# Optimization experiments

Hardware: AMD Instinct MI355X
Metric: run time of the kernel (lower is better)

## Reference

```python
import jax, jax.numpy as jnp
import numpy as np

D_MODEL = 2048
NUM_HEADS = 16
D_HEAD = D_MODEL // NUM_HEADS
ROPE_THETA = 10000.0
MAX_SEQ_LEN = 2048
NEG_INF = -1e30


def _rope_tables(seq_len):
    pos = jnp.arange(seq_len, dtype=jnp.float32)[:, None]          # [s,1]
    i = jnp.arange(0, D_HEAD, 2, dtype=jnp.float32)                 # [d/2]
    freqs = 1.0 / (ROPE_THETA ** (i / D_HEAD))
    angles = pos * freqs                                            # [s, d/2]
    return jnp.cos(angles), jnp.sin(angles)


def _apply_rope(x, cos, sin):
    # x: [b,h,s,d]; interleaved pairs: x1 = even dims, x2 = odd dims
    x1 = x[..., 0::2]
    x2 = x[..., 1::2]
    r1 = x1 * cos - x2 * sin
    r2 = x1 * sin + x2 * cos
    return jnp.stack([r1, r2], axis=-1).reshape(x.shape)


def setup_inputs() -> dict:
    key = jax.random.key(0)
    ks = jax.random.split(key, 5)
    b, s = 2, 2048
    scale = 1.0 / np.sqrt(D_MODEL)  # ~kaiming fan_in scale
    return {
        "x": jax.random.normal(ks[0], (b, s, D_MODEL), jnp.float32),
        "Wq": jax.random.normal(ks[1], (D_MODEL, D_MODEL), jnp.float32) * scale,
        "bq": jnp.zeros((D_MODEL,), jnp.float32),
        "Wk": jax.random.normal(ks[2], (D_MODEL, D_MODEL), jnp.float32) * scale,
        "bk": jnp.zeros((D_MODEL,), jnp.float32),
        "Wv": jax.random.normal(ks[3], (D_MODEL, D_MODEL), jnp.float32) * scale,
        "bv": jnp.zeros((D_MODEL,), jnp.float32),
        "Wo": jax.random.normal(ks[4], (D_MODEL, D_MODEL), jnp.float32) * scale,
        "bo": jnp.zeros((D_MODEL,), jnp.float32),
    }


def reference(x, Wq, bq, Wk, bk, Wv, bv, Wo, bo):
    b, s, _ = x.shape
    # QKV projections (torch Linear: y = x @ W.T + b)
    q = x @ Wq.T + bq
    k = x @ Wk.T + bk
    v = x @ Wv.T + bv
    # split heads: b s (h d) -> b h s d
    def split(t):
        return t.reshape(b, s, NUM_HEADS, D_HEAD).transpose(0, 2, 1, 3)
    q, k, v = split(q), split(k), split(v)
    # RoPE
    cos, sin = _rope_tables(s)
    q = _apply_rope(q, cos, sin)
    k = _apply_rope(k, cos, sin)
    # scaled dot-product attention with causal mask
    scores = jnp.einsum('bhqd,bhkd->bhqk', q, k) / jnp.sqrt(jnp.float32(D_HEAD))
    causal = jnp.tril(jnp.ones((s, s), dtype=bool))
    scores = jnp.where(causal[None, None], scores, NEG_INF)
    attn = jax.nn.softmax(scores, axis=-1)
    out = jnp.einsum('bhqk,bhkd->bhqd', attn, v)
    # merge heads and output projection
    out = out.transpose(0, 2, 1, 3).reshape(b, s, D_MODEL)
    return out @ Wo.T + bo
```

## Files before the change

kernel.cpp:

```cpp
#include <hip/hip_runtime.h>
#include <math.h>

#define D_MODEL 2048
#define NH 16
#define DH 128
#define SEQ 2048
#define NBH 32

typedef unsigned short u16;
typedef unsigned int u32;
typedef __attribute__((ext_vector_type(8))) short short8;
typedef __attribute__((ext_vector_type(4))) float floatx4;
typedef __attribute__((ext_vector_type(4))) unsigned short ushort4v;

__device__ __forceinline__ u16 f2bf(float f) {
  u32 u = __builtin_bit_cast(u32, f);
  return (u16)((u + 0x8000u) >> 16);
}
__device__ __forceinline__ float bf2f(u16 h) {
  return __builtin_bit_cast(float, (u32)h << 16);
}

__device__ __forceinline__ void async_load16(const u16* g, u16* l) {
  __builtin_amdgcn_global_load_lds(
      (const __attribute__((address_space(1))) void*)g,
      (__attribute__((address_space(3))) void*)l, 16, 0, 0);
}

template <int CTRL>
__device__ __forceinline__ float dpp_mov(float x) {
  return __builtin_bit_cast(
      float, __builtin_amdgcn_update_dpp(0, __builtin_bit_cast(int, x), CTRL,
                                         0xf, 0xf, false));
}
__device__ __forceinline__ float rmax16(float x) {
  x = fmaxf(x, dpp_mov<0x121>(x));
  x = fmaxf(x, dpp_mov<0x122>(x));
  x = fmaxf(x, dpp_mov<0x124>(x));
  x = fmaxf(x, dpp_mov<0x128>(x));
  return x;
}
__device__ __forceinline__ float radd16(float x) {
  x += dpp_mov<0x121>(x);
  x += dpp_mov<0x122>(x);
  x += dpp_mov<0x124>(x);
  x += dpp_mov<0x128>(x);
  return x;
}

__global__ void cvt_kernel(const float* __restrict__ src, u16* __restrict__ dst,
                           int n) {
  const int i = (blockIdx.x * 256 + threadIdx.x) * 8;
  if (i >= n) return;
  const floatx4 a = *(const floatx4*)(src + i);
  const floatx4 b = *(const floatx4*)(src + i + 4);
  short8 h;
  h[0] = (short)f2bf(a[0]); h[1] = (short)f2bf(a[1]);
  h[2] = (short)f2bf(a[2]); h[3] = (short)f2bf(a[3]);
  h[4] = (short)f2bf(b[0]); h[5] = (short)f2bf(b[1]);
  h[6] = (short)f2bf(b[2]); h[7] = (short)f2bf(b[3]);
  *(short8*)(dst + i) = h;
}

__global__ __launch_bounds__(256, 2) void gemm_async(
    const u16* __restrict__ A, const u16* __restrict__ W0,
    const u16* __restrict__ W1, const u16* __restrict__ W2,
    const float* __restrict__ b0, const float* __restrict__ b1,
    const float* __restrict__ b2, void* __restrict__ C0, void* __restrict__ C1,
    void* __restrict__ C2, const int qkv) {
  __shared__ u16 As[128 * 64];
  __shared__ u16 Bs[128 * 64];
  const int tid = threadIdx.x;
  const int wave = tid >> 6, lane = tid & 63;
  const int lr = lane & 15, lg = lane >> 4;
  const int m0 = blockIdx.y * 128;
  const int wm = (wave & 1) * 64, wn = (wave >> 1) * 64;

  int n0, mode;
  const u16* W;
  const float* bias;
  void* C;
  if (qkv) {
    const int which = blockIdx.x >> 4;
    n0 = (blockIdx.x & 15) * 128;
    W = which == 0 ? W0 : which == 1 ? W1 : W2;
    bias = which == 0 ? b0 : which == 1 ? b1 : b2;
    C = which == 0 ? C0 : which == 1 ? C1 : C2;
    mode = which;
  } else {
    n0 = blockIdx.x * 128;
    W = W0; bias = b0; C = C0; mode = 3;
  }

  floatx4 acc[4][4];
#pragma unroll
  for (int i = 0; i < 4; ++i)
#pragma unroll
    for (int j = 0; j < 4; ++j) {
      floatx4 z = {0.f, 0.f, 0.f, 0.f};
      acc[i][j] = z;
    }

  for (int kt = 0; kt < D_MODEL; kt += 64) {
#pragma unroll
    for (int p = 0; p < 4; ++p) {
      const int s = p * 256 + tid;
      const int row = s >> 3, c = s & 7;
      const int g = c ^ (row & 7);
      async_load16(A + (size_t)(m0 + row) * D_MODEL + kt + g * 8,
                   &As[(p * 256 + wave * 64) * 8]);
    }
#pragma unroll
    for (int p = 0; p < 4; ++p) {
      const int s = p * 256 + tid;
      const int row = s >> 3, c = s & 7;
      const int g = c ^ (row & 7);
      async_load16(W + (size_t)(n0 + row) * D_MODEL + kt + g * 8,
                   &Bs[(p * 256 + wave * 64) * 8]);
    }
    __syncthreads();

#pragma unroll
    for (int ks = 0; ks < 2; ++ks) {
      short8 af[4], bfr[4];
      const int ch = (ks * 4 + lg) ^ (lr & 7);
#pragma unroll
      for (int i = 0; i < 4; ++i)
        af[i] = *(const short8*)&As[(wm + 16 * i + lr) * 64 + ch * 8];
#pragma unroll
      for (int j = 0; j < 4; ++j)
        bfr[j] = *(const short8*)&Bs[(wn + 16 * j + lr) * 64 + ch * 8];
#pragma unroll
      for (int i = 0; i < 4; ++i)
#pragma unroll
        for (int j = 0; j < 4; ++j)
          acc[i][j] = __builtin_amdgcn_mfma_f32_16x16x32_bf16(af[i], bfr[j],
                                                              acc[i][j], 0, 0, 0);
    }
    __syncthreads();
  }

  float bj[4];
  int ncol[4];
#pragma unroll
  for (int j = 0; j < 4; ++j) {
    ncol[j] = n0 + wn + 16 * j + lr;
    bj[j] = bias[ncol[j]];
  }

  if (mode == 3) {
    float* Cf = (float*)C;
#pragma unroll
    for (int i = 0; i < 4; ++i)
#pragma unroll
      for (int r = 0; r < 4; ++r) {
        const int m = m0 + wm + 16 * i + lg * 4 + r;
#pragma unroll
        for (int j = 0; j < 4; ++j)
          Cf[(size_t)m * D_MODEL + ncol[j]] = acc[i][j][r] + bj[j];
      }
  } else if (mode == 2) {
    u16* Ch = (u16*)C;
#pragma unroll
    for (int i = 0; i < 4; ++i)
#pragma unroll
      for (int r = 0; r < 4; ++r) {
        const int m = m0 + wm + 16 * i + lg * 4 + r;
        const int b = m >> 11, s = m & (SEQ - 1);
#pragma unroll
        for (int j = 0; j < 4; ++j) {
          const int h = ncol[j] >> 7, d = ncol[j] & (DH - 1);
          Ch[((size_t)((b * NH + h) * DH + d)) * SEQ + s] =
              f2bf(acc[i][j][r] + bj[j]);
        }
      }
  } else {
    u16* Ch = (u16*)C;
#pragma unroll
    for (int i = 0; i < 4; ++i)
#pragma unroll
      for (int r = 0; r < 4; ++r) {
        const int m = m0 + wm + 16 * i + lg * 4 + r;
        const int b = m >> 11, s = m & (SEQ - 1);
#pragma unroll
        for (int j = 0; j < 4; ++j) {
          const int h = ncol[j] >> 7, d = ncol[j] & (DH - 1);
          Ch[((size_t)((b * NH + h) * SEQ + s)) * DH + d] =
              f2bf(acc[i][j][r] + bj[j]);
        }
      }
  }
}

__global__ void rope_kernel(u16* __restrict__ Q, u16* __restrict__ K) {
  const int idx = blockIdx.x * blockDim.x + threadIdx.x;
  const int p = idx & 63;
  const int s = (idx >> 6) & (SEQ - 1);
  const int bh = idx >> 17;
  if (bh >= NBH) return;
  const float freq = exp2f(-(float)p * (13.287712379549449f / 64.0f));
  const float ang = (float)s * freq;
  float sn, cs;
  sincosf(ang, &sn, &cs);
  const size_t base = ((size_t)bh * SEQ + s) * DH + 2 * p;
  {
    const u32 qq = *(const u32*)(Q + base);
    const float x1 = bf2f((u16)(qq & 0xffffu)), x2 = bf2f((u16)(qq >> 16));
    *(u32*)(Q + base) =
        (u32)f2bf(x1 * cs - x2 * sn) | ((u32)f2bf(x1 * sn + x2 * cs) << 16);
  }
  {
    const u32 kk = *(const u32*)(K + base);
    const float x1 = bf2f((u16)(kk & 0xffffu)), x2 = bf2f((u16)(kk >> 16));
    *(u32*)(K + base) =
        (u32)f2bf(x1 * cs - x2 * sn) | ((u32)f2bf(x1 * sn + x2 * cs) << 16);
  }
}

__global__ __launch_bounds__(256, 2) void attn_kernel(
    const u16* __restrict__ Q, const u16* __restrict__ K,
    const u16* __restrict__ Vt, u16* __restrict__ Oflat) {
  __shared__ u16 Ks[64 * 128];
  __shared__ u16 Vts[128 * 64];
  __shared__ u16 Ps[4 * 32 * 72];
  const int tid = threadIdx.x;
  const int wave = tid >> 6, lane = tid & 63;
  const int lr = lane & 15, lg = lane >> 4;
  const int bh = blockIdx.y;
  const int qt = (blockIdx.y < 16) ? blockIdx.x : (15 - blockIdx.x);
  const size_t qk0 = (size_t)bh * SEQ * DH;
  const int q0 = qt * 128 + wave * 32;
  const float scale = 0.08838834764831845f;
  const float L2E = 1.4426950408889634f;

  short8 qf[2][4];
#pragma unroll
  for (int i = 0; i < 2; ++i)
#pragma unroll
    for (int kb = 0; kb < 4; ++kb)
      qf[i][kb] = *(const short8*)(Q + qk0 + (size_t)(q0 + 16 * i + lr) * DH +
                                   kb * 32 + lg * 8);

  floatx4 o[2][8];
#pragma unroll
  for (int i = 0; i < 2; ++i)
#pragma unroll
    for (int jd = 0; jd < 8; ++jd) {
      floatx4 z = {0.f, 0.f, 0.f, 0.f};
      o[i][jd] = z;
    }
  float mrun[2][4], lrun[2][4];
#pragma unroll
  for (int i = 0; i < 2; ++i)
#pragma unroll
    for (int r = 0; r < 4; ++r) {
      mrun[i][r] = -1e38f;
      lrun[i][r] = 0.f;
    }

  u16* myP = &Ps[wave * 32 * 72];
  const int nkt = 2 * qt + 2;
  for (int kt = 0; kt < nkt; ++kt) {
#pragma unroll
    for (int p = 0; p < 4; ++p) {
      const int s = p * 256 + tid;
      const int row = s >> 4, c = s & 15;
      const int g = c ^ (row & 15);
      async_load16(K + qk0 + (size_t)(kt * 64 + row) * DH + g * 8,
                   &Ks[(p * 256 + wave * 64) * 8]);
    }
#pragma unroll
    for (int p = 0; p < 4; ++p) {
      const int s = p * 256 + tid;
      const int row = s >> 3, c = s & 7;
      const int g = c ^ (row & 7);
      async_load16(Vt + (size_t)bh * DH * SEQ + (size_t)row * SEQ + kt * 64 + g * 8,
                   &Vts[(p * 256 + wave * 64) * 8]);
    }
    __syncthreads();

    floatx4 sacc[2][4];
#pragma unroll
    for (int i = 0; i < 2; ++i)
#pragma unroll
      for (int j = 0; j < 4; ++j) {
        floatx4 z = {0.f, 0.f, 0.f, 0.f};
        sacc[i][j] = z;
      }
#pragma unroll
    for (int kb = 0; kb < 4; ++kb) {
      short8 kf[4];
#pragma unroll
      for (int j = 0; j < 4; ++j)
        kf[j] = *(const short8*)&Ks[(16 * j + lr) * 128 + (((kb * 4 + lg) ^ lr)) * 8];
#pragma unroll
      for (int i = 0; i < 2; ++i)
#pragma unroll
        for (int j = 0; j < 4; ++j)
          sacc[i][j] = __builtin_amdgcn_mfma_f32_16x16x32_bf16(qf[i][kb], kf[j],
                                                               sacc[i][j], 0, 0, 0);
    }

    const bool mask_tile = (kt >= 2 * qt);
#pragma unroll
    for (int i = 0; i < 2; ++i)
#pragma unroll
      for (int j = 0; j < 4; ++j)
#pragma unroll
        for (int r = 0; r < 4; ++r) {
          float v = sacc[i][j][r] * scale;
          if (mask_tile) {
            const int kpos = kt * 64 + 16 * j + lr;
            const int qpos = q0 + 16 * i + lg * 4 + r;
            if (kpos > qpos) v = -1e30f;
          }
          sacc[i][j][r] = v;
        }

    float mnew[2][4], alpha[2][4], rs[2][4];
#pragma unroll
    for (int i = 0; i < 2; ++i)
#pragma unroll
      for (int r = 0; r < 4; ++r) {
        float mx = fmaxf(fmaxf(sacc[i][0][r], sacc[i][1][r]),
                         fmaxf(sacc[i][2][r], sacc[i][3][r]));
        mx = rmax16(mx);
        const float mn = fmaxf(mrun[i][r], mx);
        mnew[i][r] = mn;
        alpha[i][r] = exp2f((mrun[i][r] - mn) * L2E);
        mrun[i][r] = mn;
        rs[i][r] = 0.f;
      }

#pragma unroll
    for (int i = 0; i < 2; ++i)
#pragma unroll
      for (int j = 0; j < 4; ++j)
#pragma unroll
        for (int r = 0; r < 4; ++r) {
          const float pv = exp2f((sacc[i][j][r] - mnew[i][r]) * L2E);
          rs[i][r] += pv;
          myP[(16 * i + lg * 4 + r) * 72 + 16 * j + lr] = f2bf(pv);
        }

#pragma unroll
    for (int i = 0; i < 2; ++i)
#pragma unroll
      for (int r = 0; r < 4; ++r)
        lrun[i][r] = lrun[i][r] * alpha[i][r] + radd16(rs[i][r]);

#pragma unroll
    for (int i = 0; i < 2; ++i)
#pragma unroll
      for (int jd = 0; jd < 8; ++jd)
#pragma unroll
        for (int r = 0; r < 4; ++r) o[i][jd][r] *= alpha[i][r];

    asm volatile("s_waitcnt lgkmcnt(0)" ::: "memory");

#pragma unroll
    for (int kb = 0; kb < 2; ++kb) {
      short8 pf[2];
#pragma unroll
      for (int i = 0; i < 2; ++i)
        pf[i] = *(const short8*)&myP[(16 * i + lr) * 72 + kb * 32 + lg * 8];
#pragma unroll
      for (int jd = 0; jd < 8; ++jd) {
        const short8 vf = *(const short8*)&Vts[(16 * jd + lr) * 64 +
                                               (((kb * 4 + lg) ^ (lr & 7))) * 8];
#pragma unroll
        for (int i = 0; i < 2; ++i)
          o[i][jd] = __builtin_amdgcn_mfma_f32_16x16x32_bf16(pf[i], vf, o[i][jd],
                                                             0, 0, 0);
      }
    }
    __syncthreads();
  }

  const int b = bh >> 4, h = bh & (NH - 1);
#pragma unroll
  for (int i = 0; i < 2; ++i)
#pragma unroll
    for (int r = 0; r < 4; ++r) {
      const int qpos = q0 + 16 * i + lg * 4 + r;
      const float inv = 1.0f / lrun[i][r];
      u16* dst = Oflat + ((size_t)(b * SEQ + qpos)) * D_MODEL + h * DH;
#pragma unroll
      for (int jd = 0; jd < 8; ++jd) dst[16 * jd + lr] = f2bf(o[i][jd][r] * inv);
    }
}

template <int ABF16>
__global__ __launch_bounds__(256, 2) void gemm_kernel(
    const void* __restrict__ Aptr, const float* __restrict__ W,
    const float* __restrict__ bias, void* __restrict__ Cptr, const int mode) {
  __shared__ u16 As[128 * 72];
  __shared__ u16 Bs[128 * 72];
  const int tid = threadIdx.x;
  const int wave = tid >> 6, lane = tid & 63;
  const int lr = lane & 15, lg = lane >> 4;
  const int m0 = blockIdx.y * 128, n0 = blockIdx.x * 128;
  const int wm = (wave & 1) * 64, wn = (wave >> 1) * 64;

  floatx4 acc[4][4];
#pragma unroll
  for (int i = 0; i < 4; ++i)
#pragma unroll
    for (int j = 0; j < 4; ++j) {
      floatx4 z = {0.f, 0.f, 0.f, 0.f};
      acc[i][j] = z;
    }

  for (int kt = 0; kt < D_MODEL; kt += 64) {
    if (ABF16) {
      const u16* A = (const u16*)Aptr;
      const int row0 = tid >> 3, c8 = (tid & 7) * 8;
#pragma unroll
      for (int p = 0; p < 4; ++p) {
        const int row = row0 + p * 32;
        *(short8*)&As[row * 72 + c8] =
            *(const short8*)(A + (size_t)(m0 + row) * D_MODEL + kt + c8);
      }
    } else {
      const float* A = (const float*)Aptr;
      const int row0 = tid >> 4, c4 = (tid & 15) * 4;
#pragma unroll
      for (int p = 0; p < 8; ++p) {
        const int row = row0 + p * 16;
        const floatx4 v =
            *(const floatx4*)(A + (size_t)(m0 + row) * D_MODEL + kt + c4);
        ushort4v h;
        h[0] = f2bf(v[0]); h[1] = f2bf(v[1]); h[2] = f2bf(v[2]); h[3] = f2bf(v[3]);
        *(ushort4v*)&As[row * 72 + c4] = h;
      }
    }
    {
      const int row0 = tid >> 4, c4 = (tid & 15) * 4;
#pragma unroll
      for (int p = 0; p < 8; ++p) {
        const int row = row0 + p * 16;
        const floatx4 v =
            *(const floatx4*)(W + (size_t)(n0 + row) * D_MODEL + kt + c4);
        ushort4v h;
        h[0] = f2bf(v[0]); h[1] = f2bf(v[1]); h[2] = f2bf(v[2]); h[3] = f2bf(v[3]);
        *(ushort4v*)&Bs[row * 72 + c4] = h;
      }
    }
    __syncthreads();
#pragma unroll
    for (int ks = 0; ks < 2; ++ks) {
      short8 af[4], bfr[4];
#pragma unroll
      for (int i = 0; i < 4; ++i)
        af[i] = *(const short8*)&As[(wm + 16 * i + lr) * 72 + ks * 32 + lg * 8];
#pragma unroll
      for (int j = 0; j < 4; ++j)
        bfr[j] = *(const short8*)&Bs[(wn + 16 * j + lr) * 72 + ks * 32 + lg * 8];
#pragma unroll
      for (int i = 0; i < 4; ++i)
#pragma unroll
        for (int j = 0; j < 4; ++j)
          acc[i][j] = __builtin_amdgcn_mfma_f32_16x16x32_bf16(af[i], bfr[j],
                                                              acc[i][j], 0, 0, 0);
    }
    __syncthreads();
  }

  float bj[4];
  int ncol[4];
#pragma unroll
  for (int j = 0; j < 4; ++j) {
    ncol[j] = n0 + wn + 16 * j + lr;
    bj[j] = bias[ncol[j]];
  }

  if (mode == 3) {
    float* C = (float*)Cptr;
#pragma unroll
    for (int i = 0; i < 4; ++i)
#pragma unroll
      for (int r = 0; r < 4; ++r) {
        const int m = m0 + wm + 16 * i + lg * 4 + r;
#pragma unroll
        for (int j = 0; j < 4; ++j)
          C[(size_t)m * D_MODEL + ncol[j]] = acc[i][j][r] + bj[j];
      }
  } else if (mode == 2) {
    u16* C = (u16*)Cptr;
#pragma unroll
    for (int i = 0; i < 4; ++i)
#pragma unroll
      for (int r = 0; r < 4; ++r) {
        const int m = m0 + wm + 16 * i + lg * 4 + r;
        const int b = m >> 11, s = m & (SEQ - 1);
#pragma unroll
        for (int j = 0; j < 4; ++j) {
          const int h = ncol[j] >> 7, d = ncol[j] & (DH - 1);
          C[((size_t)((b * NH + h) * DH + d)) * SEQ + s] = f2bf(acc[i][j][r] + bj[j]);
        }
      }
  } else {
    u16* C = (u16*)Cptr;
#pragma unroll
    for (int i = 0; i < 4; ++i)
#pragma unroll
      for (int r = 0; r < 4; ++r) {
        const int m = m0 + wm + 16 * i + lg * 4 + r;
        const int b = m >> 11, s = m & (SEQ - 1);
#pragma unroll
        for (int j = 0; j < 4; ++j) {
          const int h = ncol[j] >> 7, d = ncol[j] & (DH - 1);
          C[((size_t)((b * NH + h) * SEQ + s)) * DH + d] = f2bf(acc[i][j][r] + bj[j]);
        }
      }
  }
}

extern "C" void kernel_launch(void* const* d_in, const int* in_sizes, int n_in,
                              void* d_out, int out_size, void* d_ws,
                              size_t ws_size, hipStream_t stream) {
  const float* x = (const float*)d_in[0];
  const float* Wq = (const float*)d_in[1];
  const float* bq = (const float*)d_in[2];
  const float* Wk = (const float*)d_in[3];
  const float* bk = (const float*)d_in[4];
  const float* Wv = (const float*)d_in[5];
  const float* bv = (const float*)d_in[6];
  const float* Wo = (const float*)d_in[7];
  const float* bo = (const float*)d_in[8];
  float* out = (float*)d_out;

  const size_t E = (size_t)NBH * SEQ * DH;
  const size_t WE = (size_t)D_MODEL * D_MODEL;
  const size_t need = (4 * E + 3 * WE) * sizeof(u16);

  const dim3 gb(256);

  if (ws_size >= need) {
    u16* xb = (u16*)d_ws;
    u16* wqb = xb + E;
    u16* wkb = wqb + WE;
    u16* wvb = wkb + WE;
    u16* q = wvb + WE;
    u16* k = q + E;
    u16* vt = k + E;
    u16* aflat = xb;
    u16* wob = q;

    cvt_kernel<<<dim3((int)(E / 2048)), gb, 0, stream>>>(x, xb, (int)E);
    cvt_kernel<<<dim3((int)(WE / 2048)), gb, 0, stream>>>(Wq, wqb, (int)WE);
    cvt_kernel<<<dim3((int)(WE / 2048)), gb, 0, stream>>>(Wk, wkb, (int)WE);
    cvt_kernel<<<dim3((int)(WE / 2048)), gb, 0, stream>>>(Wv, wvb, (int)WE);

    gemm_async<<<dim3(48, 32), gb, 0, stream>>>(xb, wqb, wkb, wvb, bq, bk, bv,
                                                q, k, vt, 1);
    rope_kernel<<<dim3((NBH * SEQ * (DH / 2)) / 256), gb, 0, stream>>>(q, k);
    attn_kernel<<<dim3(SEQ / 128, NBH), gb, 0, stream>>>(q, k, vt, aflat);
    cvt_kernel<<<dim3((int)(WE / 2048)), gb, 0, stream>>>(Wo, wob, (int)WE);
    gemm_async<<<dim3(16, 32), gb, 0, stream>>>(aflat, wob, nullptr, nullptr,
                                                bo, nullptr, nullptr, out,
                                                nullptr, nullptr, 0);
  } else {
    u16* q = (u16*)d_ws;
    u16* k = q + E;
    u16* vt = k + E;
    u16* aflat = vt + E;
    const dim3 gg(D_MODEL / 128, (2 * SEQ) / 128);
    gemm_kernel<0><<<gg, gb, 0, stream>>>(x, Wq, bq, q, 0);
    gemm_kernel<0><<<gg, gb, 0, stream>>>(x, Wk, bk, k, 1);
    gemm_kernel<0><<<gg, gb, 0, stream>>>(x, Wv, bv, vt, 2);
    rope_kernel<<<dim3((NBH * SEQ * (DH / 2)) / 256), dim3(256), 0, stream>>>(q, k);
    attn_kernel<<<dim3(SEQ / 128, NBH), gb, 0, stream>>>(q, k, vt, aflat);
    gemm_kernel<1><<<gg, gb, 0, stream>>>(aflat, Wo, bo, out, 3);
  }
}
```

Before: 422.0 us.

## Compute softmax row sums via MFMA, lazy rescale, fold scale into exp2

```diff
diff --git a/kernel.cpp b/kernel.cpp
--- a/kernel.cpp
+++ b/kernel.cpp
@@ -38,13 +38,6 @@
   x = fmaxf(x, dpp_mov<0x122>(x));
   x = fmaxf(x, dpp_mov<0x124>(x));
   x = fmaxf(x, dpp_mov<0x128>(x));
-  return x;
-}
-__device__ __forceinline__ float radd16(float x) {
-  x += dpp_mov<0x121>(x);
-  x += dpp_mov<0x122>(x);
-  x += dpp_mov<0x124>(x);
-  x += dpp_mov<0x128>(x);
   return x;
 }
 
@@ -226,12 +219,14 @@
   const int tid = threadIdx.x;
   const int wave = tid >> 6, lane = tid & 63;
   const int lr = lane & 15, lg = lane >> 4;
-  const int bh = blockIdx.y;
-  const int qt = (blockIdx.y < 16) ? blockIdx.x : (15 - blockIdx.x);
+  const int L = blockIdx.y * 16 + blockIdx.x;
+  const int bh = L & 31;
+  const int t = L >> 5;
+  const int qt = (t < 8) ? t : 23 - t;
   const size_t qk0 = (size_t)bh * SEQ * DH;
   const int q0 = qt * 128 + wave * 32;
-  const float scale = 0.08838834764831845f;
-  const float L2E = 1.4426950408889634f;
+  const float C = 0.12752602f;
+  const float RTHR = 62.7f;
 
   short8 qf[2][4];
 #pragma unroll
@@ -241,22 +236,22 @@
       qf[i][kb] = *(const short8*)(Q + qk0 + (size_t)(q0 + 16 * i + lr) * DH +
                                    kb * 32 + lg * 8);
 
-  floatx4 o[2][8];
+  floatx4 o[2][9];
 #pragma unroll
   for (int i = 0; i < 2; ++i)
 #pragma unroll
-    for (int jd = 0; jd < 8; ++jd) {
+    for (int jd = 0; jd < 9; ++jd) {
       floatx4 z = {0.f, 0.f, 0.f, 0.f};
       o[i][jd] = z;
     }
-  float mrun[2][4], lrun[2][4];
+  float mrun[2][4];
 #pragma unroll
   for (int i = 0; i < 2; ++i)
 #pragma unroll
-    for (int r = 0; r < 4; ++r) {
-      mrun[i][r] = -1e38f;
-      lrun[i][r] = 0.f;
-    }
+    for (int r = 0; r < 4; ++r) mrun[i][r] = -1e38f;
+
+  const short8 onesv = {16256, 16256, 16256, 16256,
+                        16256, 16256, 16256, 16256};
 
   u16* myP = &Ps[wave * 32 * 72];
   const int nkt = 2 * qt + 2;
@@ -293,44 +288,58 @@
 #pragma unroll
       for (int j = 0; j < 4; ++j)
         kf[j] = *(const short8*)&Ks[(16 * j + lr) * 128 + (((kb * 4 + lg) ^ lr)) * 8];
+      __builtin_amdgcn_s_setprio(1);
 #pragma unroll
       for (int i = 0; i < 2; ++i)
 #pragma unroll
         for (int j = 0; j < 4; ++j)
           sacc[i][j] = __builtin_amdgcn_mfma_f32_16x16x32_bf16(qf[i][kb], kf[j],
                                                                sacc[i][j], 0, 0, 0);
-    }
-
-    const bool mask_tile = (kt >= 2 * qt);
-#pragma unroll
-    for (int i = 0; i < 2; ++i)
-#pragma unroll
-      for (int j = 0; j < 4; ++j)
-#pragma unroll
-        for (int r = 0; r < 4; ++r) {
-          float v = sacc[i][j][r] * scale;
-          if (mask_tile) {
+      __builtin_amdgcn_s_setprio(0);
+    }
+
+    if (kt >= 2 * qt) {
+#pragma unroll
+      for (int i = 0; i < 2; ++i)
+#pragma unroll
+        for (int j = 0; j < 4; ++j)
+#pragma unroll
+          for (int r = 0; r < 4; ++r) {
             const int kpos = kt * 64 + 16 * j + lr;
             const int qpos = q0 + 16 * i + lg * 4 + r;
-            if (kpos > qpos) v = -1e30f;
+            if (kpos > qpos) sacc[i][j][r] = -1e30f;
           }
-          sacc[i][j][r] = v;
+    }
+
+    float mx[2][4];
+    float g = -1e38f;
+#pragma unroll
+    for (int i = 0; i < 2; ++i)
+#pragma unroll
+      for (int r = 0; r < 4; ++r) {
+        float m = fmaxf(fmaxf(sacc[i][0][r], sacc[i][1][r]),
+                        fmaxf(sacc[i][2][r], sacc[i][3][r]));
+        m = rmax16(m);
+        mx[i][r] = m;
+        g = fmaxf(g, m - mrun[i][r]);
+      }
+    if (!__all(g <= RTHR)) {
+#pragma unroll
+      for (int i = 0; i < 2; ++i)
+#pragma unroll
+        for (int r = 0; r < 4; ++r) {
+          const float mn = fmaxf(mrun[i][r], mx[i][r]);
+          const float alpha = exp2f((mrun[i][r] - mn) * C);
+          mrun[i][r] = mn;
+#pragma unroll
+          for (int jd = 0; jd < 9; ++jd) o[i][jd][r] *= alpha;
         }
-
-    float mnew[2][4], alpha[2][4], rs[2][4];
+    }
+    float negMC[2][4];
 #pragma unroll
     for (int i = 0; i < 2; ++i)
 #pragma unroll
-      for (int r = 0; r < 4; ++r) {
-        float mx = fmaxf(fmaxf(sacc[i][0][r], sacc[i][1][r]),
-                         fmaxf(sacc[i][2][r], sacc[i][3][r]));
-        mx = rmax16(mx);
-        const float mn = fmaxf(mrun[i][r], mx);
-        mnew[i][r] = mn;
-        alpha[i][r] = exp2f((mrun[i][r] - mn) * L2E);
-        mrun[i][r] = mn;
-        rs[i][r] = 0.f;
-      }
+      for (int r = 0; r < 4; ++r) negMC[i][r] = -mrun[i][r] * C;
 
 #pragma unroll
     for (int i = 0; i < 2; ++i)
@@ -338,24 +347,10 @@
       for (int j = 0; j < 4; ++j)
 #pragma unroll
         for (int r = 0; r < 4; ++r) {
-          const float pv = exp2f((sacc[i][j][r] - mnew[i][r]) * L2E);
-          rs[i][r] += pv;
+          const float pv = exp2f(fmaf(sacc[i][j][r], C, negMC[i][r]));
           myP[(16 * i + lg * 4 + r) * 72 + 16 * j + lr] = f2bf(pv);
         }
 
-#pragma unroll
-    for (int i = 0; i < 2; ++i)
-#pragma unroll
-      for (int r = 0; r < 4; ++r)
-        lrun[i][r] = lrun[i][r] * alpha[i][r] + radd16(rs[i][r]);
-
-#pragma unroll
-    for (int i = 0; i < 2; ++i)
-#pragma unroll
-      for (int jd = 0; jd < 8; ++jd)
-#pragma unroll
-        for (int r = 0; r < 4; ++r) o[i][jd][r] *= alpha[i][r];
-
     asm volatile("s_waitcnt lgkmcnt(0)" ::: "memory");
 
 #pragma unroll
@@ -364,6 +359,7 @@
 #pragma unroll
       for (int i = 0; i < 2; ++i)
         pf[i] = *(const short8*)&myP[(16 * i + lr) * 72 + kb * 32 + lg * 8];
+      __builtin_amdgcn_s_setprio(1);
 #pragma unroll
       for (int jd = 0; jd < 8; ++jd) {
         const short8 vf = *(const short8*)&Vts[(16 * jd + lr) * 64 +
@@ -373,6 +369,11 @@
           o[i][jd] = __builtin_amdgcn_mfma_f32_16x16x32_bf16(pf[i], vf, o[i][jd],
                                                              0, 0, 0);
       }
+#pragma unroll
+      for (int i = 0; i < 2; ++i)
+        o[i][8] = __builtin_amdgcn_mfma_f32_16x16x32_bf16(pf[i], onesv, o[i][8],
+                                                          0, 0, 0);
+      __builtin_amdgcn_s_setprio(0);
     }
     __syncthreads();
   }
@@ -383,7 +384,7 @@
 #pragma unroll
     for (int r = 0; r < 4; ++r) {
       const int qpos = q0 + 16 * i + lg * 4 + r;
-      const float inv = 1.0f / lrun[i][r];
+      const float inv = 1.0f / o[i][8][r];
       u16* dst = Oflat + ((size_t)(b * SEQ + qpos)) * D_MODEL + h * DH;
 #pragma unroll
       for (int jd = 0; jd < 8; ++jd) dst[16 * jd + lr] = f2bf(o[i][jd][r] * inv);
```

Measured after the change: 395.9 us. 1.07x faster.
